# Optimization experiments

Hardware: AMD Instinct MI355X
Metric: run time of the kernel (lower is better)

Reference implementation:

```python
import jax, jax.numpy as jnp
import numpy as np

N = 50000      # nodes
E = 800000     # edges (avg degree 16)
IN = 512       # input features
OUT = 32       # per-head hidden features
H = 8          # heads (layer 1)
C = 16         # classes (layer 2, 1 head)
NEG_SLOPE = 0.2


def setup_inputs() -> dict:
    key = jax.random.key(0)
    ks = jax.random.split(key, 8)
    x = jax.random.normal(ks[0], (N, IN), jnp.float32)
    edge_index = jax.random.randint(ks[1], (2, E), 0, N, jnp.int32)
    # layer 1 params: W1 [IN, H*OUT], attention vectors a1_src/a1_dst [H, OUT]
    W1 = jax.random.normal(ks[2], (IN, H * OUT), jnp.float32) * (1.0 / np.sqrt(IN))
    a1_src = jax.random.normal(ks[3], (H, OUT), jnp.float32) * (1.0 / np.sqrt(OUT))
    a1_dst = jax.random.normal(ks[4], (H, OUT), jnp.float32) * (1.0 / np.sqrt(OUT))
    # layer 2 params: single head, W2 [H*OUT, C], a2_src/a2_dst [1, C]
    W2 = jax.random.normal(ks[5], (H * OUT, C), jnp.float32) * (1.0 / np.sqrt(H * OUT))
    a2_src = jax.random.normal(ks[6], (1, C), jnp.float32) * (1.0 / np.sqrt(C))
    a2_dst = jax.random.normal(ks[7], (1, C), jnp.float32) * (1.0 / np.sqrt(C))
    return {"x": x, "W1": W1, "a1_src": a1_src, "a1_dst": a1_dst,
            "W2": W2, "a2_src": a2_src, "a2_dst": a2_dst,
            "edge_index": edge_index}


def gat_layer(x, edge_index, W, a_src, a_dst, concat):
    """Standard GAT layer: e_ij = LeakyReLU(a_src.Wh_i + a_dst.Wh_j),
    softmax over incoming edges of each target node, scatter-aggregate."""
    n = x.shape[0]
    h_heads, f = a_src.shape
    h = (x @ W).reshape(n, h_heads, f)                      # [N, H, F]
    src, dst = edge_index[0], edge_index[1]
    es = jnp.einsum('nhf,hf->nh', h, a_src)                 # [N, H] per-node src scores
    ed = jnp.einsum('nhf,hf->nh', h, a_dst)                 # [N, H]
    e = jax.nn.leaky_relu(es[src] + ed[dst], NEG_SLOPE)     # [E, H] per-edge logits
    # segment softmax over edges grouped by dst node
    m = jax.ops.segment_max(e, dst, num_segments=n)         # [N, H]
    m = jnp.where(jnp.isfinite(m), m, 0.0)                  # empty segments -> -inf
    p = jnp.exp(e - m[dst])                                 # [E, H]
    s = jax.ops.segment_sum(p, dst, num_segments=n)         # [N, H]
    denom = s[dst]
    alpha = p / jnp.where(denom > 0, denom, 1.0)            # [E, H]
    msg = h[src] * alpha[:, :, None]                        # [E, H, F]
    out = jax.ops.segment_sum(msg, dst, num_segments=n)     # [N, H, F]
    if concat:
        return out.reshape(n, h_heads * f)
    return out.mean(axis=1)


def reference(x, W1, a1_src, a1_dst, W2, a2_src, a2_dst, edge_index):
    # dropout is identity in eval mode
    h = gat_layer(x, edge_index, W1, a1_src, a1_dst, concat=True)   # [N, H*OUT]
    h = jax.nn.elu(h)
    h = gat_layer(h, edge_index, W2, a2_src, a2_dst, concat=False)  # [N, C]
    return jax.nn.log_softmax(h, axis=1)
```

## Files before the change

### kernel.cpp

```cpp
#include <hip/hip_runtime.h>

#define NN 50000
#define EE 800000
#define KIN 512
#define HF 256
#define NH 8
#define FOUT 32
#define NC 16
#define NEG 0.2f
#define NB_SCAN 196

typedef unsigned short u16;
typedef __attribute__((ext_vector_type(8))) short shortx8;
typedef __attribute__((ext_vector_type(4))) float floatx4;
typedef __attribute__((ext_vector_type(8))) unsigned short ushortx8;
typedef __attribute__((ext_vector_type(4))) unsigned uintx4;

__device__ __forceinline__ float lrelu(float x) { return x > 0.f ? x : NEG * x; }

__device__ __forceinline__ u16 f2bf(float f) {
    unsigned u = __float_as_uint(f);
    return (u16)((u + 0x7FFFu + ((u >> 16) & 1u)) >> 16);
}
__device__ __forceinline__ float bf2f(u16 v) {
    return __uint_as_float((unsigned)v << 16);
}
__device__ __forceinline__ unsigned pk2bf(float a, float b) {
    unsigned ua = __float_as_uint(a), ub = __float_as_uint(b);
    return ((ua + 0x8000u) >> 16) | ((ub + 0x8000u) & 0xffff0000u);
}

__device__ __forceinline__ void gll16(const void* g, void* l) {
    __builtin_amdgcn_global_load_lds((const __attribute__((address_space(1))) void*)g,
                                     (__attribute__((address_space(3))) void*)l, 16, 0, 0);
}

__global__ void count_deg_convw(const int* __restrict__ dst, int* __restrict__ deg,
                                const float* __restrict__ W1, const float* __restrict__ W2,
                                u16* __restrict__ w1t, u16* __restrict__ w2t) {
    int e = blockIdx.x * 256 + threadIdx.x;
    if (e < EE) atomicAdd(&deg[dst[e]], 1);
    if (e < KIN * HF) {
        int k = e >> 8, n = e & 255;
        w1t[n * KIN + k] = f2bf(W1[e]);
    } else if (e < KIN * HF + HF * NC) {
        int e2 = e - KIN * HF;
        int k = e2 >> 4, c = e2 & 15;
        w2t[c * HF + k] = f2bf(W2[e2]);
    }
}

__global__ __launch_bounds__(256) void scan_a(const int* __restrict__ deg, int* __restrict__ bsum) {
    __shared__ int sm[256];
    int t = threadIdx.x;
    int i = blockIdx.x * 256 + t;
    sm[t] = (i < NN) ? deg[i] : 0;
    __syncthreads();
    for (int o = 128; o; o >>= 1) { if (t < o) sm[t] += sm[t + o]; __syncthreads(); }
    if (t == 0) bsum[blockIdx.x] = sm[0];
}

__global__ __launch_bounds__(256) void scan_c(const int* __restrict__ deg, const int* __restrict__ bsum,
                                              int* __restrict__ off) {
    __shared__ int sm[256];
    __shared__ int pre[256];
    int t = threadIdx.x;
    pre[t] = (t < blockIdx.x && t < NB_SCAN) ? bsum[t] : 0;
    __syncthreads();
    for (int o = 128; o; o >>= 1) { if (t < o) pre[t] += pre[t + o]; __syncthreads(); }
    int bofs = pre[0];
    __syncthreads();
    int i = blockIdx.x * 256 + t;
    int d = (i < NN) ? deg[i] : 0;
    sm[t] = d;
    __syncthreads();
    for (int dd = 1; dd < 256; dd <<= 1) {
        int v = (t >= dd) ? sm[t - dd] : 0;
        __syncthreads();
        sm[t] += v;
        __syncthreads();
    }
    if (i < NN) off[i] = bofs + sm[t] - d;
    if (i == 0) off[NN] = EE;
}

__global__ void fill_csr(const int* __restrict__ src, const int* __restrict__ dst,
                         const int* __restrict__ off, int* __restrict__ cursor,
                         int* __restrict__ csr_src) {
    int e = blockIdx.x * 256 + threadIdx.x;
    if (e < EE) {
        int d = dst[e];
        int pos = atomicAdd(&cursor[d], 1);
        csr_src[off[d] + pos] = src[e];
    }
}

__global__ __launch_bounds__(256, 2) void gemm1_mfma(const float* __restrict__ x,
                                                     const u16* __restrict__ w1t,
                                                     u16* __restrict__ h1b,
                                                     const float* __restrict__ a1s,
                                                     const float* __restrict__ a1d,
                                                     float* __restrict__ es1,
                                                     float* __restrict__ ed1) {
    __shared__ __align__(16) float As[128 * 32];
    __shared__ __align__(16) u16 Bs[256 * 32];
    int t = threadIdx.x;
    int lane = t & 63, wave = t >> 6;
    int wm = wave >> 1, wn = wave & 1;
    int lm = lane & 15, quad = lane >> 4;
    int bm = blockIdx.x * 128;

    floatx4 acc[4][8];
#pragma unroll
    for (int i = 0; i < 4; i++)
#pragma unroll
        for (int j = 0; j < 8; j++) acc[i][j] = (floatx4){0.f, 0.f, 0.f, 0.f};

    int arow_l = wave * 32 + (lane >> 3);
    int akoff = (lane & 7) * 4;
    const float* aptr[4];
#pragma unroll
    for (int i = 0; i < 4; i++) {
        int ar = bm + arow_l + i * 8;
        if (ar > NN - 1) ar = NN - 1;
        aptr[i] = x + (size_t)ar * KIN + akoff;
    }
    float* alds[4];
#pragma unroll
    for (int i = 0; i < 4; i++) alds[i] = As + (wave * 32 + i * 8) * 32;

    int brow_l = wave * 64 + (lane >> 2);
    int bkoff = (lane & 3) * 8;
    const u16* bptr[4];
#pragma unroll
    for (int i = 0; i < 4; i++) bptr[i] = w1t + (size_t)(brow_l + i * 16) * KIN + bkoff;
    u16* blds[4];
#pragma unroll
    for (int i = 0; i < 4; i++) blds[i] = Bs + (wave * 64 + i * 16) * 32;

    int offA[4], offB[8];
#pragma unroll
    for (int i = 0; i < 4; i++) offA[i] = (wm * 64 + i * 16 + lm) * 32 + quad * 8;
#pragma unroll
    for (int j = 0; j < 8; j++) offB[j] = (wn * 128 + j * 16 + lm) * 32 + quad * 8;

    for (int kk = 0; kk < KIN; kk += 32) {
#pragma unroll
        for (int i = 0; i < 4; i++) gll16(aptr[i] + kk, alds[i]);
#pragma unroll
        for (int i = 0; i < 4; i++) gll16(bptr[i] + kk, blds[i]);
        __syncthreads();
        shortx8 af[4], bf[8];
#pragma unroll
        for (int i = 0; i < 4; i++) {
            const float4* ap = (const float4*)&As[offA[i]];
            float4 lo = ap[0], hi = ap[1];
            union { uintx4 u; shortx8 s; } cv;
            cv.u[0] = pk2bf(lo.x, lo.y);
            cv.u[1] = pk2bf(lo.z, lo.w);
            cv.u[2] = pk2bf(hi.x, hi.y);
            cv.u[3] = pk2bf(hi.z, hi.w);
            af[i] = cv.s;
        }
#pragma unroll
        for (int j = 0; j < 8; j++) bf[j] = *(const shortx8*)&Bs[offB[j]];
#pragma unroll
        for (int i = 0; i < 4; i++)
#pragma unroll
            for (int j = 0; j < 8; j++)
                acc[i][j] = __builtin_amdgcn_mfma_f32_16x16x32_bf16(af[i], bf[j], acc[i][j], 0, 0, 0);
        __syncthreads();
    }

#pragma unroll
    for (int i = 0; i < 4; i++) {
        int row = bm + wm * 64 + i * 16 + quad * 4;
#pragma unroll
        for (int j = 0; j < 8; j++) {
            int col = wn * 128 + j * 16 + lm;
#pragma unroll
            for (int r = 0; r < 4; r++) {
                if (row + r < NN) h1b[(size_t)(row + r) * HF + col] = f2bf(acc[i][j][r]);
            }
        }
    }

    float as_v[8], ad_v[8];
#pragma unroll
    for (int j = 0; j < 8; j++) {
        int col = wn * 128 + j * 16 + lm;
        as_v[j] = a1s[col];
        ad_v[j] = a1d[col];
    }
#pragma unroll
    for (int i = 0; i < 4; i++) {
#pragma unroll
        for (int r = 0; r < 4; r++) {
            int row = bm + wm * 64 + i * 16 + quad * 4 + r;
#pragma unroll
            for (int hp = 0; hp < 4; hp++) {
                float e_s = acc[i][2 * hp][r] * as_v[2 * hp] + acc[i][2 * hp + 1][r] * as_v[2 * hp + 1];
                float e_d = acc[i][2 * hp][r] * ad_v[2 * hp] + acc[i][2 * hp + 1][r] * ad_v[2 * hp + 1];
#pragma unroll
                for (int o = 8; o; o >>= 1) {
                    e_s += __shfl_down(e_s, o, 16);
                    e_d += __shfl_down(e_d, o, 16);
                }
                if (lm == 0 && row < NN) {
                    int h = wn * 4 + hp;
                    es1[row * NH + h] = e_s;
                    ed1[row * NH + h] = e_d;
                }
            }
        }
    }
}

__global__ __launch_bounds__(256) void agg1(const u16* __restrict__ h1b, const float* __restrict__ es,
                                            const float* __restrict__ ed, const int* __restrict__ off,
                                            const int* __restrict__ csr_src, u16* __restrict__ out1b) {
    int wave = threadIdx.x >> 6;
    int lane = threadIdx.x & 63;
    int n = blockIdx.x * 4 + wave;
    int fh = lane & 31;
    int ep = lane >> 5;
    int head = fh >> 2;
    int beg = off[n];
    int deg = off[n + 1] - beg;
    float edh = ed[n * NH + head];
    const u16* hbase = h1b + fh * 8;
    float acc[8] = {0.f, 0.f, 0.f, 0.f, 0.f, 0.f, 0.f, 0.f};
    float s_part = 0.f;
    for (int base = 0; base < deg; base += 16) {
        int nch = deg - base; if (nch > 16) nch = 16;
        int sv = (lane < nch) ? csr_src[beg + base + lane] : 0;
#pragma unroll
        for (int e = 0; e < 8; e++) {
            int ee = 2 * e + ep;
            int s = __shfl(sv, ee, 64);
            if (ee < nch) {
                float lg = es[s * NH + head] + edh;
                float p = __expf(lg > 0.f ? lg : NEG * lg);
                ushortx8 hv = *(const ushortx8*)(hbase + (size_t)s * HF);
                s_part += p;
#pragma unroll
                for (int i = 0; i < 8; i++) acc[i] += p * bf2f(hv[i]);
            }
        }
    }
#pragma unroll
    for (int i = 0; i < 8; i++) acc[i] += __shfl_down(acc[i], 32, 64);
    s_part += __shfl_down(s_part, 32, 64);
    if (lane < 32) {
        float inv = s_part > 0.f ? 1.0f / s_part : 0.f;
        union { uintx4 u; ushortx8 v; } ob;
#pragma unroll
        for (int i = 0; i < 4; i++) {
            float v0 = acc[2 * i] * inv, v1 = acc[2 * i + 1] * inv;
            v0 = v0 > 0.f ? v0 : (__expf(v0) - 1.0f);
            v1 = v1 > 0.f ? v1 : (__expf(v1) - 1.0f);
            ob.u[i] = (unsigned)f2bf(v0) | ((unsigned)f2bf(v1) << 16);
        }
        *(ushortx8*)(out1b + (size_t)n * HF + fh * 8) = ob.v;
    }
}

__global__ __launch_bounds__(64) void gemm2_mfma(const u16* __restrict__ out1b, const u16* __restrict__ w2t,
                                                 const float* __restrict__ a2s, const float* __restrict__ a2d,
                                                 u16* __restrict__ h2b, float* __restrict__ es2,
                                                 float* __restrict__ ed2) {
    int lane = threadIdx.x;
    int lm = lane & 15, quad = lane >> 4;
    int nb = blockIdx.x * 16;
    floatx4 acc = (floatx4){0.f, 0.f, 0.f, 0.f};
    const u16* arow = out1b + (size_t)(nb + lm) * HF + quad * 8;
    const u16* brow = w2t + lm * HF + quad * 8;
#pragma unroll
    for (int kk = 0; kk < HF; kk += 32) {
        shortx8 af = *(const shortx8*)(arow + kk);
        shortx8 bf = *(const shortx8*)(brow + kk);
        acc = __builtin_amdgcn_mfma_f32_16x16x32_bf16(af, bf, acc, 0, 0, 0);
    }
    float a2sc = a2s[lm], a2dc = a2d[lm];
#pragma unroll
    for (int r = 0; r < 4; r++) {
        int n = nb + quad * 4 + r;
        float v = acc[r];
        h2b[n * NC + lm] = f2bf(v);
        float ps = v * a2sc, pd = v * a2dc;
#pragma unroll
        for (int o = 8; o; o >>= 1) {
            ps += __shfl_down(ps, o, 16);
            pd += __shfl_down(pd, o, 16);
        }
        if (lm == 0) { es2[n] = ps; ed2[n] = pd; }
    }
}

__global__ __launch_bounds__(256) void agg2(const u16* __restrict__ h2b, const float* __restrict__ es2,
                                            const float* __restrict__ ed2, const int* __restrict__ off,
                                            const int* __restrict__ csr_src, float* __restrict__ out) {
    int t = threadIdx.x;
    int nid = blockIdx.x * 16 + (t >> 4);
    int c = t & 15;
    int beg = off[nid];
    int deg = off[nid + 1] - beg;
    float edn = ed2[nid];
    float s = 0.f, acc = 0.f;
    for (int base = 0; base < deg; base += 16) {
        int nch = deg - base; if (nch > 16) nch = 16;
        int sv = 0;
        if (c < nch) sv = csr_src[beg + base + c];
        int sva[16];
#pragma unroll
        for (int e = 0; e < 16; e++) sva[e] = __shfl(sv, e, 16);
        float hva[16];
#pragma unroll
        for (int e = 0; e < 16; e++) hva[e] = bf2f(h2b[sva[e] * NC + c]);
        float p = 0.f;
        if (c < nch) p = __expf(lrelu(es2[sv] + edn));
        s += p;
        float pa[16];
#pragma unroll
        for (int e = 0; e < 16; e++) pa[e] = __shfl(p, e, 16);
#pragma unroll
        for (int e = 0; e < 16; e++) acc += pa[e] * hva[e];
    }
#pragma unroll
    for (int o = 8; o; o >>= 1) s += __shfl_down(s, o, 16);
    s = __shfl(s, 0, 16);
    float v = (s > 0.f) ? acc / s : 0.f;
    float m2 = v;
#pragma unroll
    for (int o = 8; o; o >>= 1) m2 = fmaxf(m2, __shfl_down(m2, o, 16));
    m2 = __shfl(m2, 0, 16);
    float se = __expf(v - m2);
#pragma unroll
    for (int o = 8; o; o >>= 1) se += __shfl_down(se, o, 16);
    se = __shfl(se, 0, 16);
    out[nid * NC + c] = v - m2 - __logf(se);
}

extern "C" void kernel_launch(void* const* d_in, const int* in_sizes, int n_in,
                              void* d_out, int out_size, void* d_ws, size_t ws_size,
                              hipStream_t stream) {
    const float* x   = (const float*)d_in[0];
    const float* W1  = (const float*)d_in[1];
    const float* a1s = (const float*)d_in[2];
    const float* a1d = (const float*)d_in[3];
    const float* W2  = (const float*)d_in[4];
    const float* a2s = (const float*)d_in[5];
    const float* a2d = (const float*)d_in[6];
    const int*   ei  = (const int*)d_in[7];
    const int* srcv = ei;
    const int* dstv = ei + EE;
    float* out = (float*)d_out;

    u16* h1b    = (u16*)d_ws;
    u16* out1b  = h1b + (size_t)NN * HF;
    float* es1  = (float*)(out1b + (size_t)NN * HF);
    float* ed1  = es1 + (size_t)NN * NH;
    u16* h2b    = (u16*)(ed1 + (size_t)NN * NH);
    float* es2v = (float*)(h2b + (size_t)NN * NC);
    float* ed2v = es2v + NN;
    int* deg    = (int*)(ed2v + NN);
    int* cursor = deg + NN;
    int* offs   = cursor + NN;
    int* csr    = offs + NN + 1;
    int* bsum   = csr + EE;
    u16* w1t    = (u16*)(bsum + 256);
    u16* w2t    = w1t + (size_t)HF * KIN;

    hipMemsetAsync(deg, 0, 2 * NN * sizeof(int), stream);
    count_deg_convw<<<(EE + 255) / 256, 256, 0, stream>>>(dstv, deg, W1, W2, w1t, w2t);
    scan_a<<<NB_SCAN, 256, 0, stream>>>(deg, bsum);
    scan_c<<<NB_SCAN, 256, 0, stream>>>(deg, bsum, offs);
    fill_csr<<<(EE + 255) / 256, 256, 0, stream>>>(srcv, dstv, offs, cursor, csr);
    gemm1_mfma<<<(NN + 127) / 128, 256, 0, stream>>>(x, w1t, h1b, a1s, a1d, es1, ed1);
    agg1<<<NN / 4, 256, 0, stream>>>(h1b, es1, ed1, offs, csr, out1b);
    gemm2_mfma<<<NN / 16, 64, 0, stream>>>(out1b, w2t, a2s, a2d, h2b, es2v, ed2v);
    agg2<<<NN / 16, 256, 0, stream>>>(h2b, es2v, ed2v, offs, csr, out);
}
```

Before: 359.2 us.

## Rewrite layer-1 aggregation as block-level MFMA over 16-node edge chunks

Replaces the per-node wave gather-and-FMA aggregation with a block that handles 16 consecutive destination nodes. Source rows for 32-edge chunks are staged into LDS with async global-to-LDS loads under an XOR swizzle. The kernel builds a masked attention-probability matrix (edge to local destination) in bf16 and computes both the weighted sums and the softmax denominators with MFMA. This trades scalar FMAs and poor per-node occupancy for matrix-core work and coalesced staging. It adds two block syncs per chunk, rounds the probabilities to bf16, and wastes MFMA lanes on zeros in the mask.

```diff
diff --git a/kernel.cpp b/kernel.cpp
--- a/kernel.cpp
+++ b/kernel.cpp
@@ -216,52 +216,127 @@
     }
 }
 
-__global__ __launch_bounds__(256) void agg1(const u16* __restrict__ h1b, const float* __restrict__ es,
-                                            const float* __restrict__ ed, const int* __restrict__ off,
-                                            const int* __restrict__ csr_src, u16* __restrict__ out1b) {
-    int wave = threadIdx.x >> 6;
-    int lane = threadIdx.x & 63;
-    int n = blockIdx.x * 4 + wave;
-    int fh = lane & 31;
-    int ep = lane >> 5;
-    int head = fh >> 2;
-    int beg = off[n];
-    int deg = off[n + 1] - beg;
-    float edh = ed[n * NH + head];
-    const u16* hbase = h1b + fh * 8;
-    float acc[8] = {0.f, 0.f, 0.f, 0.f, 0.f, 0.f, 0.f, 0.f};
-    float s_part = 0.f;
-    for (int base = 0; base < deg; base += 16) {
-        int nch = deg - base; if (nch > 16) nch = 16;
-        int sv = (lane < nch) ? csr_src[beg + base + lane] : 0;
-#pragma unroll
-        for (int e = 0; e < 8; e++) {
-            int ee = 2 * e + ep;
-            int s = __shfl(sv, ee, 64);
-            if (ee < nch) {
-                float lg = es[s * NH + head] + edh;
-                float p = __expf(lg > 0.f ? lg : NEG * lg);
-                ushortx8 hv = *(const ushortx8*)(hbase + (size_t)s * HF);
-                s_part += p;
-#pragma unroll
-                for (int i = 0; i < 8; i++) acc[i] += p * bf2f(hv[i]);
+__global__ __launch_bounds__(256) void agg1_mfma(const u16* __restrict__ h1b, const float* __restrict__ es,
+                                                 const float* __restrict__ ed, const int* __restrict__ off,
+                                                 const int* __restrict__ csr_src, u16* __restrict__ out1b) {
+    __shared__ __align__(16) u16 Hs[32 * 256];
+    __shared__ __align__(16) u16 pTs[8][32];
+    __shared__ __align__(16) unsigned char dstloc[32];
+    __shared__ int offs_s[17];
+    __shared__ float ed_s[16][8];
+
+    int t = threadIdx.x;
+    int lane = t & 63, wave = t >> 6;
+    int lm = lane & 15, quad = lane >> 4;
+    int base = blockIdx.x * 16;
+
+    if (t < 17) offs_s[t] = off[base + t];
+    if (t < 128) ed_s[t >> 3][t & 7] = ed[(base + (t >> 3)) * NH + (t & 7)];
+    int e0 = off[base];
+    int e1 = off[base + 16];
+    int nch = (e1 - e0 + 31) >> 5;
+    __syncthreads();
+
+    floatx4 acc[2][2];
+    floatx4 accS[2];
+#pragma unroll
+    for (int a = 0; a < 2; a++) {
+        accS[a] = (floatx4){0.f, 0.f, 0.f, 0.f};
+#pragma unroll
+        for (int b = 0; b < 2; b++) acc[a][b] = (floatx4){0.f, 0.f, 0.f, 0.f};
+    }
+
+    int h0 = 2 * wave;
+    shortx8 ones;
+#pragma unroll
+    for (int i = 0; i < 8; i++) ones[i] = (short)0x3F80;
+
+    int k_p = t >> 3, h_p = t & 7;
+    int sv = 0;
+    if (nch > 0) {
+        int g = e0 + (lane & 31);
+        sv = csr_src[g < e1 ? g : e1 - 1];
+    }
+
+    for (int c = 0; c < nch; c++) {
+        int svn = 0;
+        if (c + 1 < nch) {
+            int g = e0 + ((c + 1) << 5) + (lane & 31);
+            svn = csr_src[g < e1 ? g : e1 - 1];
+        }
+#pragma unroll
+        for (int pass = 0; pass < 4; pass++) {
+            int r = pass * 8 + 2 * wave + (lane >> 5);
+            int s = __shfl(sv, r, 64);
+            const u16* sp = h1b + (size_t)s * HF + (((lane & 31) ^ (pass << 1)) << 3);
+            gll16(sp, Hs + pass * 2048 + wave * 512);
+        }
+        {
+            int g = e0 + (c << 5) + k_p;
+            int s = __shfl(sv, k_p, 64);
+            float pv = 0.f;
+            if (g < e1) {
+                int m = 0;
+                if (offs_s[m + 8] <= g) m += 8;
+                if (offs_s[m + 4] <= g) m += 4;
+                if (offs_s[m + 2] <= g) m += 2;
+                if (offs_s[m + 1] <= g) m += 1;
+                float lg = es[s * NH + h_p] + ed_s[m][h_p];
+                lg = lg > 0.f ? lg : NEG * lg;
+                pv = __expf(lg);
+                if (h_p == 0) dstloc[k_p] = (unsigned char)m;
             }
-        }
-    }
-#pragma unroll
-    for (int i = 0; i < 8; i++) acc[i] += __shfl_down(acc[i], 32, 64);
-    s_part += __shfl_down(s_part, 32, 64);
-    if (lane < 32) {
-        float inv = s_part > 0.f ? 1.0f / s_part : 0.f;
-        union { uintx4 u; ushortx8 v; } ob;
-#pragma unroll
-        for (int i = 0; i < 4; i++) {
-            float v0 = acc[2 * i] * inv, v1 = acc[2 * i + 1] * inv;
-            v0 = v0 > 0.f ? v0 : (__expf(v0) - 1.0f);
-            v1 = v1 > 0.f ? v1 : (__expf(v1) - 1.0f);
-            ob.u[i] = (unsigned)f2bf(v0) | ((unsigned)f2bf(v1) << 16);
-        }
-        *(ushortx8*)(out1b + (size_t)n * HF + fh * 8) = ob.v;
+            pTs[h_p][k_p] = f2bf(pv);
+        }
+        __syncthreads();
+
+        union { uintx4 u; shortx8 s; } pa, pb, a0, a1;
+        pa.s = *(const shortx8*)&pTs[h0][quad * 8];
+        pb.s = *(const shortx8*)&pTs[h0 + 1][quad * 8];
+        unsigned dw0 = *(const unsigned*)&dstloc[quad * 8];
+        unsigned dw1 = *(const unsigned*)&dstloc[quad * 8 + 4];
+        unsigned ulm = (unsigned)lm;
+        unsigned mm0 = ((dw0 & 255u) == ulm ? 0xffffu : 0u) | (((dw0 >> 8) & 255u) == ulm ? 0xffff0000u : 0u);
+        unsigned mm1 = (((dw0 >> 16) & 255u) == ulm ? 0xffffu : 0u) | ((dw0 >> 24) == ulm ? 0xffff0000u : 0u);
+        unsigned mm2 = ((dw1 & 255u) == ulm ? 0xffffu : 0u) | (((dw1 >> 8) & 255u) == ulm ? 0xffff0000u : 0u);
+        unsigned mm3 = (((dw1 >> 16) & 255u) == ulm ? 0xffffu : 0u) | ((dw1 >> 24) == ulm ? 0xffff0000u : 0u);
+        a0.u[0] = pa.u[0] & mm0; a0.u[1] = pa.u[1] & mm1; a0.u[2] = pa.u[2] & mm2; a0.u[3] = pa.u[3] & mm3;
+        a1.u[0] = pb.u[0] & mm0; a1.u[1] = pb.u[1] & mm1; a1.u[2] = pb.u[2] & mm2; a1.u[3] = pb.u[3] & mm3;
+
+        accS[0] = __builtin_amdgcn_mfma_f32_16x16x32_bf16(a0.s, ones, accS[0], 0, 0, 0);
+        accS[1] = __builtin_amdgcn_mfma_f32_16x16x32_bf16(a1.s, ones, accS[1], 0, 0, 0);
+
+#pragma unroll
+        for (int hh = 0; hh < 2; hh++) {
+#pragma unroll
+            for (int half = 0; half < 2; half++) {
+                int f = (h0 + hh) * 32 + half * 16 + lm;
+                int bidx = (quad * 8) * 256 + (((f >> 3) ^ (quad << 1)) << 3) + (f & 7);
+                shortx8 bfv;
+#pragma unroll
+                for (int j = 0; j < 8; j++) bfv[j] = (short)Hs[bidx + j * 256];
+                acc[hh][half] = __builtin_amdgcn_mfma_f32_16x16x32_bf16(
+                    hh ? a1.s : a0.s, bfv, acc[hh][half], 0, 0, 0);
+            }
+        }
+        __syncthreads();
+        sv = svn;
+    }
+
+#pragma unroll
+    for (int hh = 0; hh < 2; hh++) {
+#pragma unroll
+        for (int r = 0; r < 4; r++) {
+            float sden = accS[hh][r];
+            float inv = sden > 0.f ? 1.0f / sden : 0.f;
+            int n = base + quad * 4 + r;
+#pragma unroll
+            for (int half = 0; half < 2; half++) {
+                float v = acc[hh][half][r] * inv;
+                v = v > 0.f ? v : (__expf(v) - 1.0f);
+                out1b[(size_t)n * HF + (h0 + hh) * 32 + half * 16 + lm] = f2bf(v);
+            }
+        }
     }
 }
 
@@ -377,7 +452,7 @@
     scan_c<<<NB_SCAN, 256, 0, stream>>>(deg, bsum, offs);
     fill_csr<<<(EE + 255) / 256, 256, 0, stream>>>(srcv, dstv, offs, cursor, csr);
     gemm1_mfma<<<(NN + 127) / 128, 256, 0, stream>>>(x, w1t, h1b, a1s, a1d, es1, ed1);
-    agg1<<<NN / 4, 256, 0, stream>>>(h1b, es1, ed1, offs, csr, out1b);
+    agg1_mfma<<<NN / 16, 256, 0, stream>>>(h1b, es1, ed1, offs, csr, out1b);
     gemm2_mfma<<<NN / 16, 64, 0, stream>>>(out1b, w2t, a2s, a2d, h2b, es2v, ed2v);
     agg2<<<NN / 16, 256, 0, stream>>>(h2b, es2v, ed2v, offs, csr, out);
 }
```

Measured after the change: 360.3 us. No clear change (+0.3%).
